# Optimization experiments

Hardware: AMD Instinct MI355X
Metric: run time of the kernel (lower is better)

The kernel has to match this reference:

```python
import jax, jax.numpy as jnp
import numpy as np

V, E, EH, H = 32000, 512, 1024, 512  # vocab, emb_dim, enc_hidden, dec_hidden
B, S = 16, 128


def setup_inputs() -> dict:
    key = jax.random.key(0)
    ks = jax.random.split(key, 8)
    g = lambda k, shape, scale: (jax.random.normal(k, shape, jnp.float32) * scale)
    return {
        "y": jax.random.randint(ks[0], (B, S), 0, V),
        "hn": jax.random.normal(ks[1], (B, 1, EH), jnp.float32),
        "emb": g(ks[2], (V, E), 0.02),          # embedding table
        "W_ih": g(ks[3], (3 * H, E), 0.05),      # GRU input weights (r,z,n)
        "W_hh": g(ks[4], (3 * H, H), 0.05),      # GRU hidden weights (r,z,n)
        "b_ih": jnp.zeros((3 * H,), jnp.float32),
        "b_hh": jnp.zeros((3 * H,), jnp.float32),
        "fc_w": g(ks[5], (H, EH), 0.03),         # fc: enc_hidden -> dec_hidden
        "fc_b": jnp.zeros((H,), jnp.float32),
        "pred_w": g(ks[6], (V, H), 0.03),        # pred: dec_hidden -> vocab
        "pred_b": jnp.zeros((V,), jnp.float32),
    }


def gru_scan(x, h0, W_ih, W_hh, b_ih, b_hh):
    """Single-layer unidirectional GRU (PyTorch gate order r,z,n).
    x: [B,S,E], h0: [B,H] -> outputs [B,S,H]."""
    h_dim = h0.shape[-1]
    # precompute input projections for all timesteps: [B,S,3H]
    gx = jnp.einsum('bse,ge->bsg', x, W_ih) + b_ih
    Wr, Wz, Wn = W_hh[:h_dim], W_hh[h_dim:2 * h_dim], W_hh[2 * h_dim:]
    br, bz, bn = b_hh[:h_dim], b_hh[h_dim:2 * h_dim], b_hh[2 * h_dim:]

    def step(h, g):
        gr, gz, gn = g[:, :h_dim], g[:, h_dim:2 * h_dim], g[:, 2 * h_dim:]
        r = jax.nn.sigmoid(gr + h @ Wr.T + br)
        z = jax.nn.sigmoid(gz + h @ Wz.T + bz)
        n = jnp.tanh(gn + r * (h @ Wn.T + bn))
        h_new = (1.0 - z) * n + z * h
        return h_new, h_new

    _, outs = jax.lax.scan(step, h0, jnp.swapaxes(gx, 0, 1))  # [S,B,H]
    return jnp.swapaxes(outs, 0, 1)  # [B,S,H]


def reference(y, hn, emb, W_ih, W_hh, b_ih, b_hh, fc_w, fc_b, pred_w, pred_b):
    # hn: [B,1,EH] -> fc -> [B,1,H] -> permute(1,0,2) -> initial hidden [B,H]
    h0 = (hn @ fc_w.T + fc_b)[:, 0, :]
    x = emb[y]  # [B,S,E]; dropout is identity in eval mode
    out = gru_scan(x, h0, W_ih, W_hh, b_ih, b_hh)  # [B,S,H]
    return out @ pred_w.T + pred_b  # [B,S,V]
```

## Files before the change

### kernel.cpp

```cpp
#include <hip/hip_runtime.h>


typedef __attribute__((ext_vector_type(8))) short           bf8_t;
typedef __attribute__((ext_vector_type(8))) unsigned short  us8_t;
typedef __attribute__((ext_vector_type(4))) unsigned short  us4_t;
typedef __attribute__((ext_vector_type(4))) float           f4_t;
typedef __attribute__((ext_vector_type(4))) unsigned int    u4_t;

#define SENT 0xFFFFFFFFu

__device__ __forceinline__ unsigned short f2bf(float x) {
    unsigned u = __builtin_bit_cast(unsigned, x);
    u += 0x7FFFu + ((u >> 16) & 1u);
    return (unsigned short)(u >> 16);
}
__device__ __forceinline__ float fsigm(float x) {
    return __builtin_amdgcn_rcpf(1.f + __expf(-x));
}
__device__ __forceinline__ float ftanh(float x) {
    float e = __expf(2.f * x);
    return 1.f - 2.f * __builtin_amdgcn_rcpf(e + 1.f);
}

__device__ __forceinline__ bf8_t mk_frag(f4_t v0, f4_t v1) {
    bf8_t f;
    f[0] = (short)f2bf(v0[0]); f[1] = (short)f2bf(v0[1]);
    f[2] = (short)f2bf(v0[2]); f[3] = (short)f2bf(v0[3]);
    f[4] = (short)f2bf(v1[0]); f[5] = (short)f2bf(v1[1]);
    f[6] = (short)f2bf(v1[2]); f[7] = (short)f2bf(v1[3]);
    return f;
}

__device__ __forceinline__ void llc_store_u32(unsigned int* p, unsigned int v) {
    asm volatile("global_store_dword %0, %1, off sc0 sc1" :: "v"(p), "v"(v) : "memory");
}

__global__ void k_fill(unsigned int* __restrict__ hbuf, unsigned int* __restrict__ hout,
                       int* __restrict__ ticket) {
    if (blockIdx.x == 0 && threadIdx.x == 0) *ticket = 0;
    int i = blockIdx.x * blockDim.x + threadIdx.x;
    u4_t v = {SENT, SENT, SENT, SENT};
    if (i < 132096) ((u4_t*)hbuf)[i] = v;
    else            ((u4_t*)hout)[i - 132096] = v;
}

__global__ void k_conv(const float* __restrict__ src, unsigned short* __restrict__ dst, int n4) {
    int i = blockIdx.x * blockDim.x + threadIdx.x;
    int stride = gridDim.x * blockDim.x;
    for (; i < n4; i += stride) {
        f4_t v = ((const f4_t*)src)[i];
        us4_t o;
        o[0] = f2bf(v[0]); o[1] = f2bf(v[1]); o[2] = f2bf(v[2]); o[3] = f2bf(v[3]);
        ((us4_t*)dst)[i] = o;
    }
}

__global__ void k_gather(const int* __restrict__ y, const float* __restrict__ emb,
                         unsigned short* __restrict__ xbf) {
    int m = blockIdx.x;
    int row = y[m];
    int t = threadIdx.x;
    f4_t v = ((const f4_t*)(emb + (size_t)row * 512))[t];
    us4_t o;
    o[0] = f2bf(v[0]); o[1] = f2bf(v[1]); o[2] = f2bf(v[2]); o[3] = f2bf(v[3]);
    ((us4_t*)(xbf + (size_t)m * 512))[t] = o;
}

__global__ void k_h0(const float* __restrict__ hn, const float* __restrict__ fc_w,
                     const float* __restrict__ fc_b, float* __restrict__ h0m) {
    __shared__ float sh[1024];
    int b = blockIdx.x, t = threadIdx.x;
    for (int i = t; i < 1024; i += 256) sh[i] = hn[b * 1024 + i];
    __syncthreads();
    int j = t;
    float a0 = fc_b[j], a1 = fc_b[j + 256];
    const float* w0 = fc_w + (size_t)j * 1024;
    const float* w1 = fc_w + (size_t)(j + 256) * 1024;
    #pragma unroll 8
    for (int e = 0; e < 1024; e++) { float he = sh[e]; a0 += he * w0[e]; a1 += he * w1[e]; }
    h0m[b * 512 + j] = a0;
    h0m[b * 512 + j + 256] = a1;
}

__launch_bounds__(256)
__global__ void k_gemm(const unsigned short* __restrict__ A, const unsigned short* __restrict__ Bt,
                       const float* __restrict__ bias, float* __restrict__ C, int N) {
    __shared__ unsigned short sA[128 * 64];
    __shared__ unsigned short sB[128 * 64];
    const int m0 = blockIdx.y * 128, n0 = blockIdx.x * 128;
    const int tid = threadIdx.x, lane = tid & 63, wave = tid >> 6;
    const int wm = wave >> 1, wn = wave & 1;
    f4_t acc[4][4] = {};
    for (int ks = 0; ks < 8; ks++) {
        const int k0 = ks * 64;
        #pragma unroll
        for (int t = 0; t < 4; t++) {
            int idx = tid + t * 256;
            int row = idx >> 3, slot = idx & 7;
            int sw = ((slot ^ (row & 7)) << 3);
            *(us8_t*)(&sA[row * 64 + sw]) = *(const us8_t*)(A + (size_t)(m0 + row) * 512 + k0 + slot * 8);
            *(us8_t*)(&sB[row * 64 + sw]) = *(const us8_t*)(Bt + (size_t)(n0 + row) * 512 + k0 + slot * 8);
        }
        __syncthreads();
        #pragma unroll
        for (int kk = 0; kk < 2; kk++) {
            bf8_t af[4], bfr[4];
            #pragma unroll
            for (int mi = 0; mi < 4; mi++) {
                int row = wm * 64 + mi * 16 + (lane & 15);
                int slot = (kk * 4 + (lane >> 4)) ^ (row & 7);
                af[mi] = *(const bf8_t*)(&sA[row * 64 + slot * 8]);
            }
            #pragma unroll
            for (int ni = 0; ni < 4; ni++) {
                int row = wn * 64 + ni * 16 + (lane & 15);
                int slot = (kk * 4 + (lane >> 4)) ^ (row & 7);
                bfr[ni] = *(const bf8_t*)(&sB[row * 64 + slot * 8]);
            }
            #pragma unroll
            for (int mi = 0; mi < 4; mi++)
                #pragma unroll
                for (int ni = 0; ni < 4; ni++)
                    acc[mi][ni] = __builtin_amdgcn_mfma_f32_16x16x32_bf16(af[mi], bfr[ni], acc[mi][ni], 0, 0, 0);
        }
        __syncthreads();
    }
    #pragma unroll
    for (int ni = 0; ni < 4; ni++) {
        int col = n0 + wn * 64 + ni * 16 + (lane & 15);
        float bv = bias[col];
        #pragma unroll
        for (int mi = 0; mi < 4; mi++) {
            int rbase = m0 + wm * 64 + mi * 16 + (lane >> 4) * 4;
            #pragma unroll
            for (int r = 0; r < 4; r++)
                C[(size_t)(rbase + r) * N + col] = acc[mi][ni][r] + bv;
        }
    }
}

__launch_bounds__(256, 1)
__global__ void k_fused(const float* __restrict__ W_hh, const float* __restrict__ b_hh,
                        const float* __restrict__ gx, const float* __restrict__ h0m,
                        unsigned int* __restrict__ hbuf, unsigned int* __restrict__ HoutP,
                        const unsigned short* __restrict__ pwbf, const float* __restrict__ pred_b,
                        float* __restrict__ out, int* __restrict__ tticket) {
    __shared__ __align__(16) unsigned char smem[32768];
    __shared__ int s_tile;
    const int tid = threadIdx.x;
    const int lane = tid & 63;
    const int wave = tid >> 6;

    if (blockIdx.x < 16) {
        float* sPart = (float*)smem;
        const int c = blockIdx.x;
        const int ch = wave >> 1, w = wave & 1;
        const int col = c * 32 + ch * 16 + (lane & 15);
        const int kgrp = lane >> 4, bbase = kgrp * 4;

        bf8_t wfR[8], wfZ[8], wfN[8];
        {
            const f4_t* wr = (const f4_t*)(W_hh + (size_t)col * 512);
            const f4_t* wz = (const f4_t*)(W_hh + (size_t)(512 + col) * 512);
            const f4_t* wn = (const f4_t*)(W_hh + (size_t)(1024 + col) * 512);
            const int fo = kgrp * 2;
            #pragma unroll
            for (int j = 0; j < 8; j++) {
                const int kk = w * 8 + j;
                wfR[j] = mk_frag(wr[kk * 8 + fo], wr[kk * 8 + fo + 1]);
                wfZ[j] = mk_frag(wz[kk * 8 + fo], wz[kk * 8 + fo + 1]);
                wfN[j] = mk_frag(wn[kk * 8 + fo], wn[kk * 8 + fo + 1]);
            }
        }
        float brv = 0.f, bzv = 0.f, bnv = 0.f;
        f4_t h_reg = {0.f, 0.f, 0.f, 0.f};
        if (w == 0) {
            brv = b_hh[col]; bzv = b_hh[512 + col]; bnv = b_hh[1024 + col];
            #pragma unroll
            for (int r = 0; r < 4; r++) h_reg[r] = h0m[(bbase + r) * 512 + col];
            #pragma unroll
            for (int r = 0; r < 4; r++) {
                unsigned int hb = f2bf(h_reg[r]);
                unsigned int pr = __shfl_xor(hb, 1, 64);
                if (!(lane & 1))
                    llc_store_u32(&hbuf[(bbase + r) * 256 + (col >> 1)], hb | (pr << 16));
            }
        }

        for (int s = 1; s <= 128; s++) {
            float gxr[4], gxz[4], gxn[4];
            if (w == 0) {
                #pragma unroll
                for (int r = 0; r < 4; r++) {
                    const float* gp = gx + (size_t)((bbase + r) * 128 + (s - 1)) * 1536 + col;
                    gxr[r] = gp[0]; gxz[r] = gp[512]; gxn[r] = gp[1024];
                }
            }
            const unsigned int* base = hbuf + (size_t)(s - 1) * 4096
                                     + (lane & 15) * 256 + kgrp * 4 + w * 128;
            u4_t q[8];
            int spins = 0;
            bool ok;
            do {
                asm volatile(
                    "global_load_dwordx4 %0, %8, off sc0 sc1\n\t"
                    "global_load_dwordx4 %1, %8, off offset:64 sc0 sc1\n\t"
                    "global_load_dwordx4 %2, %8, off offset:128 sc0 sc1\n\t"
                    "global_load_dwordx4 %3, %8, off offset:192 sc0 sc1\n\t"
                    "global_load_dwordx4 %4, %8, off offset:256 sc0 sc1\n\t"
                    "global_load_dwordx4 %5, %8, off offset:320 sc0 sc1\n\t"
                    "global_load_dwordx4 %6, %8, off offset:384 sc0 sc1\n\t"
                    "global_load_dwordx4 %7, %8, off offset:448 sc0 sc1\n\t"
                    "s_waitcnt vmcnt(0)"
                    : "=&v"(q[0]), "=&v"(q[1]), "=&v"(q[2]), "=&v"(q[3]),
                      "=&v"(q[4]), "=&v"(q[5]), "=&v"(q[6]), "=&v"(q[7])
                    : "v"(base)
                    : "memory");
                ok = true;
                #pragma unroll
                for (int j = 0; j < 8; j++)
                    #pragma unroll
                    for (int i = 0; i < 4; i++)
                        ok = ok && (q[j][i] != SENT);
            } while (!__all(ok) && ++spins < (1 << 20));
            __builtin_amdgcn_sched_barrier(0);

            f4_t aR = {}, aZ = {}, aN = {};
            #pragma unroll
            for (int j = 0; j < 8; j++) {
                bf8_t af = __builtin_bit_cast(bf8_t, q[j]);
                aR = __builtin_amdgcn_mfma_f32_16x16x32_bf16(af, wfR[j], aR, 0, 0, 0);
                aZ = __builtin_amdgcn_mfma_f32_16x16x32_bf16(af, wfZ[j], aZ, 0, 0, 0);
                aN = __builtin_amdgcn_mfma_f32_16x16x32_bf16(af, wfN[j], aN, 0, 0, 0);
            }

            const int slot = s & 1;
            if (w == 1) {
                #pragma unroll
                for (int r = 0; r < 4; r++) {
                    sPart[((slot * 2 + ch) * 12 + r) * 64 + lane]     = aR[r];
                    sPart[((slot * 2 + ch) * 12 + 4 + r) * 64 + lane] = aZ[r];
                    sPart[((slot * 2 + ch) * 12 + 8 + r) * 64 + lane] = aN[r];
                }
            }
            __syncthreads();
            if (w == 0) {
                unsigned int hb[4];
                #pragma unroll
                for (int r = 0; r < 4; r++) {
                    float pR = aR[r] + sPart[((slot * 2 + ch) * 12 + r) * 64 + lane];
                    float pZ = aZ[r] + sPart[((slot * 2 + ch) * 12 + 4 + r) * 64 + lane];
                    float pN = aN[r] + sPart[((slot * 2 + ch) * 12 + 8 + r) * 64 + lane];
                    float rr = fsigm(gxr[r] + pR + brv);
                    float zz = fsigm(gxz[r] + pZ + bzv);
                    float nn = ftanh(gxn[r] + rr * (pN + bnv));
                    float hnew = (1.f - zz) * nn + zz * h_reg[r];
                    h_reg[r] = hnew;
                    hb[r] = f2bf(hnew);
                }
                #pragma unroll
                for (int r = 0; r < 4; r++) {
                    unsigned int pr = __shfl_xor(hb[r], 1, 64);
                    if (!(lane & 1))
                        llc_store_u32(&hbuf[(size_t)s * 4096 + (bbase + r) * 256 + (col >> 1)],
                                      hb[r] | (pr << 16));
                }
                #pragma unroll
                for (int r = 0; r < 4; r++) {
                    unsigned int pr = __shfl_xor(hb[r], 1, 64);
                    if (!(lane & 1))
                        llc_store_u32(&HoutP[(size_t)((s - 1) * 16 + bbase + r) * 256 + (col >> 1)],
                                      hb[r] | (pr << 16));
                }
            }
        }
        __syncthreads();
    }

    unsigned short* sA = (unsigned short*)smem;
    unsigned short* sB = sA + 8192;
    const int wm = wave >> 1, wn = wave & 1;
    const unsigned short* A = (const unsigned short*)HoutP;

    int rowA[4], slotA[4];
    #pragma unroll
    for (int t4 = 0; t4 < 4; t4++) {
        int idx = tid + t4 * 256;
        rowA[t4] = idx >> 3; slotA[t4] = idx & 7;
    }

    for (;;) {
        if (tid == 0) s_tile = atomicAdd(tticket, 1);
        __syncthreads();
        const int t = s_tile;
        __syncthreads();
        if (t >= 4000) break;
        const int tm = t / 250, tn = t - tm * 250;
        const int m0 = tm * 128, n0 = tn * 128;

        if (tid == 0) {
            const unsigned int* probe = HoutP + (size_t)(m0 + 127) * 256 + 255;
            unsigned v; int guard = 0;
            do {
                asm volatile("global_load_dword %0, %1, off sc0 sc1\n\ts_waitcnt vmcnt(0)"
                             : "=&v"(v) : "v"(probe) : "memory");
                if (v == SENT) __builtin_amdgcn_s_sleep(16);
            } while (v == SENT && ++guard < (1 << 20));
        }
        __syncthreads();

        f4_t acc[4][4] = {};
        for (int ks = 0; ks < 8; ks++) {
            const int k0 = ks * 64;
            #pragma unroll
            for (int t4 = 0; t4 < 4; t4++) {
                int row = rowA[t4], slot = slotA[t4];
                int sw = ((slot ^ (row & 7)) << 3);
                *(us8_t*)(&sB[row * 64 + sw]) =
                    *(const us8_t*)(pwbf + (size_t)(n0 + row) * 512 + k0 + slot * 8);
            }
            {
                const unsigned short* p0 = A + (size_t)(m0 + rowA[0]) * 512 + k0 + slotA[0] * 8;
                const unsigned short* p1 = A + (size_t)(m0 + rowA[1]) * 512 + k0 + slotA[1] * 8;
                const unsigned short* p2 = A + (size_t)(m0 + rowA[2]) * 512 + k0 + slotA[2] * 8;
                const unsigned short* p3 = A + (size_t)(m0 + rowA[3]) * 512 + k0 + slotA[3] * 8;
                u4_t a0, a1, a2, a3;
                int spins = 0; bool okk;
                do {
                    asm volatile(
                        "global_load_dwordx4 %0, %4, off sc0 sc1\n\t"
                        "global_load_dwordx4 %1, %5, off sc0 sc1\n\t"
                        "global_load_dwordx4 %2, %6, off sc0 sc1\n\t"
                        "global_load_dwordx4 %3, %7, off sc0 sc1\n\t"
                        "s_waitcnt vmcnt(0)"
                        : "=&v"(a0), "=&v"(a1), "=&v"(a2), "=&v"(a3)
                        : "v"(p0), "v"(p1), "v"(p2), "v"(p3)
                        : "memory");
                    okk = true;
                    #pragma unroll
                    for (int i = 0; i < 4; i++)
                        okk = okk && (a0[i] != SENT) && (a1[i] != SENT)
                                  && (a2[i] != SENT) && (a3[i] != SENT);
                    if (!okk) __builtin_amdgcn_s_sleep(1);
                } while (!okk && ++spins < (1 << 20));
                __builtin_amdgcn_sched_barrier(0);
                *(u4_t*)(&sA[rowA[0] * 64 + ((slotA[0] ^ (rowA[0] & 7)) << 3)]) = a0;
                *(u4_t*)(&sA[rowA[1] * 64 + ((slotA[1] ^ (rowA[1] & 7)) << 3)]) = a1;
                *(u4_t*)(&sA[rowA[2] * 64 + ((slotA[2] ^ (rowA[2] & 7)) << 3)]) = a2;
                *(u4_t*)(&sA[rowA[3] * 64 + ((slotA[3] ^ (rowA[3] & 7)) << 3)]) = a3;
            }
            __syncthreads();
            #pragma unroll
            for (int kk = 0; kk < 2; kk++) {
                bf8_t af[4], bfr[4];
                #pragma unroll
                for (int mi = 0; mi < 4; mi++) {
                    int row = wm * 64 + mi * 16 + (lane & 15);
                    int slot = (kk * 4 + (lane >> 4)) ^ (row & 7);
                    af[mi] = *(const bf8_t*)(&sA[row * 64 + slot * 8]);
                }
                #pragma unroll
                for (int ni = 0; ni < 4; ni++) {
                    int row = wn * 64 + ni * 16 + (lane & 15);
                    int slot = (kk * 4 + (lane >> 4)) ^ (row & 7);
                    bfr[ni] = *(const bf8_t*)(&sB[row * 64 + slot * 8]);
                }
                #pragma unroll
                for (int mi = 0; mi < 4; mi++)
                    #pragma unroll
                    for (int ni = 0; ni < 4; ni++)
                        acc[mi][ni] = __builtin_amdgcn_mfma_f32_16x16x32_bf16(af[mi], bfr[ni], acc[mi][ni], 0, 0, 0);
            }
            __syncthreads();
        }
        #pragma unroll
        for (int ni = 0; ni < 4; ni++) {
            int colI = n0 + wn * 64 + ni * 16 + (lane & 15);
            float bv = pred_b[colI];
            #pragma unroll
            for (int mi = 0; mi < 4; mi++) {
                int rbase = m0 + wm * 64 + mi * 16 + (lane >> 4) * 4;
                #pragma unroll
                for (int r = 0; r < 4; r++) {
                    int mr = rbase + r;
                    out[(size_t)((mr & 15) * 128 + (mr >> 4)) * 32000 + colI] = acc[mi][ni][r] + bv;
                }
            }
        }
    }
}

extern "C" void kernel_launch(void* const* d_in, const int* in_sizes, int n_in,
                              void* d_out, int out_size, void* d_ws, size_t ws_size,
                              hipStream_t stream) {
    const int*   y      = (const int*)  d_in[0];
    const float* hn     = (const float*)d_in[1];
    const float* emb    = (const float*)d_in[2];
    const float* W_ih   = (const float*)d_in[3];
    const float* W_hh   = (const float*)d_in[4];
    const float* b_ih   = (const float*)d_in[5];
    const float* b_hh   = (const float*)d_in[6];
    const float* fc_w   = (const float*)d_in[7];
    const float* fc_b   = (const float*)d_in[8];
    const float* pred_w = (const float*)d_in[9];
    const float* pred_b = (const float*)d_in[10];
    float* out = (float*)d_out;

    char* ws = (char*)d_ws;
    size_t off = 0;
    auto alloc = [&](size_t bytes) { void* p = ws + off; off = (off + bytes + 255) & ~(size_t)255; return p; };
    unsigned int*   hbuf   = (unsigned int*)   alloc((size_t)129 * 4096 * 4);
    unsigned int*   HoutP  = (unsigned int*)   alloc((size_t)2048 * 256 * 4);
    int*            tticket= (int*)            alloc(256);
    float*          h0m    = (float*)          alloc((size_t)16 * 512 * 4);
    float*          gx     = (float*)          alloc((size_t)2048 * 1536 * 4);
    unsigned short* xbf    = (unsigned short*) alloc((size_t)2048 * 512 * 2);
    unsigned short* wihbf  = (unsigned short*) alloc((size_t)1536 * 512 * 2);
    unsigned short* pwbf   = (unsigned short*) alloc((size_t)32000 * 512 * 2);
    (void)ws_size; (void)in_sizes; (void)n_in; (void)out_size;

    k_fill  <<<1028, 256, 0, stream>>>(hbuf, HoutP, tticket);
    k_conv  <<<4096, 256, 0, stream>>>(pred_w, pwbf, 32000 * 512 / 4);
    k_conv  <<<512,  256, 0, stream>>>(W_ih,  wihbf, 1536 * 512 / 4);
    k_gather<<<2048, 128, 0, stream>>>(y, emb, xbf);
    k_h0    <<<16,   256, 0, stream>>>(hn, fc_w, fc_b, h0m);
    dim3 gG(12, 16);
    k_gemm  <<<gG, 256, 0, stream>>>(xbf, wihbf, b_ih, gx, 1536);
    k_fused <<<256, 256, 0, stream>>>(W_hh, b_hh, gx, h0m, hbuf, HoutP,
                                      pwbf, pred_b, out, tticket);
}
```

Baseline: 645.0 us.

## Keep prediction weight panels resident in LDS with static panel-per-block scheduling

Replaces the atomic-ticket tile scheduler for the vocab projection with a static assignment: each of the 240 non-recurrent blocks owns one 128-column panel of the bf16 prediction weights. It loads the full 128x512 panel into a 128KB LDS buffer once, then walks the 16 row tiles in order as the GRU publishes hidden states. This removes the repeated reloading of pred_w for every row tile. The ten blocks that own two panels must reload them every row tile, so those blocks carry a heavier tail. The recurrent blocks now exit instead of joining the GEMM, and LDS use grows to 144KB per block.

```diff
diff --git a/kernel.cpp b/kernel.cpp
--- a/kernel.cpp
+++ b/kernel.cpp
@@ -35,9 +35,7 @@
     asm volatile("global_store_dword %0, %1, off sc0 sc1" :: "v"(p), "v"(v) : "memory");
 }
 
-__global__ void k_fill(unsigned int* __restrict__ hbuf, unsigned int* __restrict__ hout,
-                       int* __restrict__ ticket) {
-    if (blockIdx.x == 0 && threadIdx.x == 0) *ticket = 0;
+__global__ void k_fill(unsigned int* __restrict__ hbuf, unsigned int* __restrict__ hout) {
     int i = blockIdx.x * blockDim.x + threadIdx.x;
     u4_t v = {SENT, SENT, SENT, SENT};
     if (i < 132096) ((u4_t*)hbuf)[i] = v;
@@ -144,9 +142,8 @@
                         const float* __restrict__ gx, const float* __restrict__ h0m,
                         unsigned int* __restrict__ hbuf, unsigned int* __restrict__ HoutP,
                         const unsigned short* __restrict__ pwbf, const float* __restrict__ pred_b,
-                        float* __restrict__ out, int* __restrict__ tticket) {
-    __shared__ __align__(16) unsigned char smem[32768];
-    __shared__ int s_tile;
+                        float* __restrict__ out) {
+    __shared__ __align__(16) unsigned char smem[131072 + 16384];
     const int tid = threadIdx.x;
     const int lane = tid & 63;
     const int wave = tid >> 6;
@@ -274,13 +271,16 @@
                 }
             }
         }
-        __syncthreads();
-    }
-
-    unsigned short* sA = (unsigned short*)smem;
-    unsigned short* sB = sA + 8192;
+        return;
+    }
+
+    unsigned short* sBp = (unsigned short*)smem;
+    unsigned short* sA  = (unsigned short*)(smem + 131072);
     const int wm = wave >> 1, wn = wave & 1;
     const unsigned short* A = (const unsigned short*)HoutP;
+
+    const int tnA = blockIdx.x - 16;
+    const int npan = (tnA < 10) ? 2 : 1;
 
     int rowA[4], slotA[4];
     #pragma unroll
@@ -289,15 +289,8 @@
         rowA[t4] = idx >> 3; slotA[t4] = idx & 7;
     }
 
-    for (;;) {
-        if (tid == 0) s_tile = atomicAdd(tticket, 1);
-        __syncthreads();
-        const int t = s_tile;
-        __syncthreads();
-        if (t >= 4000) break;
-        const int tm = t / 250, tn = t - tm * 250;
-        const int m0 = tm * 128, n0 = tn * 128;
-
+    for (int tm = 0; tm < 16; tm++) {
+        const int m0 = tm * 128;
         if (tid == 0) {
             const unsigned int* probe = HoutP + (size_t)(m0 + 127) * 256 + 255;
             unsigned v; int guard = 0;
@@ -309,81 +302,90 @@
         }
         __syncthreads();
 
-        f4_t acc[4][4] = {};
-        for (int ks = 0; ks < 8; ks++) {
-            const int k0 = ks * 64;
-            #pragma unroll
-            for (int t4 = 0; t4 < 4; t4++) {
-                int row = rowA[t4], slot = slotA[t4];
-                int sw = ((slot ^ (row & 7)) << 3);
-                *(us8_t*)(&sB[row * 64 + sw]) =
-                    *(const us8_t*)(pwbf + (size_t)(n0 + row) * 512 + k0 + slot * 8);
-            }
-            {
-                const unsigned short* p0 = A + (size_t)(m0 + rowA[0]) * 512 + k0 + slotA[0] * 8;
-                const unsigned short* p1 = A + (size_t)(m0 + rowA[1]) * 512 + k0 + slotA[1] * 8;
-                const unsigned short* p2 = A + (size_t)(m0 + rowA[2]) * 512 + k0 + slotA[2] * 8;
-                const unsigned short* p3 = A + (size_t)(m0 + rowA[3]) * 512 + k0 + slotA[3] * 8;
-                u4_t a0, a1, a2, a3;
-                int spins = 0; bool okk;
-                do {
-                    asm volatile(
-                        "global_load_dwordx4 %0, %4, off sc0 sc1\n\t"
-                        "global_load_dwordx4 %1, %5, off sc0 sc1\n\t"
-                        "global_load_dwordx4 %2, %6, off sc0 sc1\n\t"
-                        "global_load_dwordx4 %3, %7, off sc0 sc1\n\t"
-                        "s_waitcnt vmcnt(0)"
-                        : "=&v"(a0), "=&v"(a1), "=&v"(a2), "=&v"(a3)
-                        : "v"(p0), "v"(p1), "v"(p2), "v"(p3)
-                        : "memory");
-                    okk = true;
+        for (int pi = 0; pi < npan; pi++) {
+            const int tn = (pi == 0) ? tnA : 240 + tnA;
+            const int n0 = tn * 128;
+
+            if (tm == 0 || npan == 2) {
+                #pragma unroll
+                for (int t4 = 0; t4 < 32; t4++) {
+                    int idx = tid + t4 * 256;
+                    int row = idx >> 6, slot = idx & 63;
+                    *(us8_t*)(&sBp[row * 512 + ((slot ^ (row & 7)) << 3)]) =
+                        *(const us8_t*)(pwbf + (size_t)(n0 + row) * 512 + slot * 8);
+                }
+            }
+            __syncthreads();
+
+            f4_t acc[4][4] = {};
+            for (int ks = 0; ks < 8; ks++) {
+                const int k0 = ks * 64;
+                {
+                    const unsigned short* p0 = A + (size_t)(m0 + rowA[0]) * 512 + k0 + slotA[0] * 8;
+                    const unsigned short* p1 = A + (size_t)(m0 + rowA[1]) * 512 + k0 + slotA[1] * 8;
+                    const unsigned short* p2 = A + (size_t)(m0 + rowA[2]) * 512 + k0 + slotA[2] * 8;
+                    const unsigned short* p3 = A + (size_t)(m0 + rowA[3]) * 512 + k0 + slotA[3] * 8;
+                    u4_t a0, a1, a2, a3;
+                    int spins = 0; bool okk;
+                    do {
+                        asm volatile(
+                            "global_load_dwordx4 %0, %4, off sc0 sc1\n\t"
+                            "global_load_dwordx4 %1, %5, off sc0 sc1\n\t"
+                            "global_load_dwordx4 %2, %6, off sc0 sc1\n\t"
+                            "global_load_dwordx4 %3, %7, off sc0 sc1\n\t"
+                            "s_waitcnt vmcnt(0)"
+                            : "=&v"(a0), "=&v"(a1), "=&v"(a2), "=&v"(a3)
+                            : "v"(p0), "v"(p1), "v"(p2), "v"(p3)
+                            : "memory");
+                        okk = true;
+                        #pragma unroll
+                        for (int i = 0; i < 4; i++)
+                            okk = okk && (a0[i] != SENT) && (a1[i] != SENT)
+                                      && (a2[i] != SENT) && (a3[i] != SENT);
+                        if (!okk) __builtin_amdgcn_s_sleep(1);
+                    } while (!okk && ++spins < (1 << 20));
+                    __builtin_amdgcn_sched_barrier(0);
+                    *(u4_t*)(&sA[rowA[0] * 64 + ((slotA[0] ^ (rowA[0] & 7)) << 3)]) = a0;
+                    *(u4_t*)(&sA[rowA[1] * 64 + ((slotA[1] ^ (rowA[1] & 7)) << 3)]) = a1;
+                    *(u4_t*)(&sA[rowA[2] * 64 + ((slotA[2] ^ (rowA[2] & 7)) << 3)]) = a2;
+                    *(u4_t*)(&sA[rowA[3] * 64 + ((slotA[3] ^ (rowA[3] & 7)) << 3)]) = a3;
+                }
+                __syncthreads();
+                #pragma unroll
+                for (int kk = 0; kk < 2; kk++) {
+                    bf8_t af[4], bfr[4];
                     #pragma unroll
-                    for (int i = 0; i < 4; i++)
-                        okk = okk && (a0[i] != SENT) && (a1[i] != SENT)
-                                  && (a2[i] != SENT) && (a3[i] != SENT);
-                    if (!okk) __builtin_amdgcn_s_sleep(1);
-                } while (!okk && ++spins < (1 << 20));
-                __builtin_amdgcn_sched_barrier(0);
-                *(u4_t*)(&sA[rowA[0] * 64 + ((slotA[0] ^ (rowA[0] & 7)) << 3)]) = a0;
-                *(u4_t*)(&sA[rowA[1] * 64 + ((slotA[1] ^ (rowA[1] & 7)) << 3)]) = a1;
-                *(u4_t*)(&sA[rowA[2] * 64 + ((slotA[2] ^ (rowA[2] & 7)) << 3)]) = a2;
-                *(u4_t*)(&sA[rowA[3] * 64 + ((slotA[3] ^ (rowA[3] & 7)) << 3)]) = a3;
-            }
-            __syncthreads();
-            #pragma unroll
-            for (int kk = 0; kk < 2; kk++) {
-                bf8_t af[4], bfr[4];
+                    for (int mi = 0; mi < 4; mi++) {
+                        int row = wm * 64 + mi * 16 + (lane & 15);
+                        int slot = (kk * 4 + (lane >> 4)) ^ (row & 7);
+                        af[mi] = *(const bf8_t*)(&sA[row * 64 + slot * 8]);
+                    }
+                    #pragma unroll
+                    for (int ni = 0; ni < 4; ni++) {
+                        int row = wn * 64 + ni * 16 + (lane & 15);
+                        int slot = (ks * 8 + kk * 4 + (lane >> 4)) ^ (row & 7);
+                        bfr[ni] = *(const bf8_t*)(&sBp[row * 512 + slot * 8]);
+                    }
+                    #pragma unroll
+                    for (int mi = 0; mi < 4; mi++)
+                        #pragma unroll
+                        for (int ni = 0; ni < 4; ni++)
+                            acc[mi][ni] = __builtin_amdgcn_mfma_f32_16x16x32_bf16(af[mi], bfr[ni], acc[mi][ni], 0, 0, 0);
+                }
+                __syncthreads();
+            }
+            #pragma unroll
+            for (int ni = 0; ni < 4; ni++) {
+                int colI = n0 + wn * 64 + ni * 16 + (lane & 15);
+                float bv = pred_b[colI];
                 #pragma unroll
                 for (int mi = 0; mi < 4; mi++) {
-                    int row = wm * 64 + mi * 16 + (lane & 15);
-                    int slot = (kk * 4 + (lane >> 4)) ^ (row & 7);
-                    af[mi] = *(const bf8_t*)(&sA[row * 64 + slot * 8]);
-                }
-                #pragma unroll
-                for (int ni = 0; ni < 4; ni++) {
-                    int row = wn * 64 + ni * 16 + (lane & 15);
-                    int slot = (kk * 4 + (lane >> 4)) ^ (row & 7);
-                    bfr[ni] = *(const bf8_t*)(&sB[row * 64 + slot * 8]);
-                }
-                #pragma unroll
-                for (int mi = 0; mi < 4; mi++)
+                    int rbase = m0 + wm * 64 + mi * 16 + (lane >> 4) * 4;
                     #pragma unroll
-                    for (int ni = 0; ni < 4; ni++)
-                        acc[mi][ni] = __builtin_amdgcn_mfma_f32_16x16x32_bf16(af[mi], bfr[ni], acc[mi][ni], 0, 0, 0);
-            }
-            __syncthreads();
-        }
-        #pragma unroll
-        for (int ni = 0; ni < 4; ni++) {
-            int colI = n0 + wn * 64 + ni * 16 + (lane & 15);
-            float bv = pred_b[colI];
-            #pragma unroll
-            for (int mi = 0; mi < 4; mi++) {
-                int rbase = m0 + wm * 64 + mi * 16 + (lane >> 4) * 4;
-                #pragma unroll
-                for (int r = 0; r < 4; r++) {
-                    int mr = rbase + r;
-                    out[(size_t)((mr & 15) * 128 + (mr >> 4)) * 32000 + colI] = acc[mi][ni][r] + bv;
+                    for (int r = 0; r < 4; r++) {
+                        int mr = rbase + r;
+                        out[(size_t)((mr & 15) * 128 + (mr >> 4)) * 32000 + colI] = acc[mi][ni][r] + bv;
+                    }
                 }
             }
         }
@@ -411,7 +413,6 @@
     auto alloc = [&](size_t bytes) { void* p = ws + off; off = (off + bytes + 255) & ~(size_t)255; return p; };
     unsigned int*   hbuf   = (unsigned int*)   alloc((size_t)129 * 4096 * 4);
     unsigned int*   HoutP  = (unsigned int*)   alloc((size_t)2048 * 256 * 4);
-    int*            tticket= (int*)            alloc(256);
     float*          h0m    = (float*)          alloc((size_t)16 * 512 * 4);
     float*          gx     = (float*)          alloc((size_t)2048 * 1536 * 4);
     unsigned short* xbf    = (unsigned short*) alloc((size_t)2048 * 512 * 2);
@@ -419,7 +420,7 @@
     unsigned short* pwbf   = (unsigned short*) alloc((size_t)32000 * 512 * 2);
     (void)ws_size; (void)in_sizes; (void)n_in; (void)out_size;
 
-    k_fill  <<<1028, 256, 0, stream>>>(hbuf, HoutP, tticket);
+    k_fill  <<<1028, 256, 0, stream>>>(hbuf, HoutP);
     k_conv  <<<4096, 256, 0, stream>>>(pred_w, pwbf, 32000 * 512 / 4);
     k_conv  <<<512,  256, 0, stream>>>(W_ih,  wihbf, 1536 * 512 / 4);
     k_gather<<<2048, 128, 0, stream>>>(y, emb, xbf);
@@ -427,5 +428,5 @@
     dim3 gG(12, 16);
     k_gemm  <<<gG, 256, 0, stream>>>(xbf, wihbf, b_ih, gx, 1536);
     k_fused <<<256, 256, 0, stream>>>(W_hh, b_hh, gx, h0m, hbuf, HoutP,
-                                      pwbf, pred_b, out, tticket);
-}
+                                      pwbf, pred_b, out);
+}
```

New measurement: 695.8 us. +7.9%, slower.
